# Kernel tuning notes

Measured on AMD Instinct MI355X. Metric: run time of the kernel, lower is better.

## Reference

```python
import jax, jax.numpy as jnp
import numpy as np

B, T, NODES, D = 8, 32, 400, 64   # batch graphs, time steps, stocks, node_feat_dim==lstm_dim
N = B * T * NODES                 # 102400 total nodes
E = 1_638_400                     # edges (avg degree 16)
L1, L2, FC1, FC2 = 96, 64, 128, 3

def setup_inputs() -> dict:
    key = jax.random.key(0)
    ks = jax.random.split(key, 12)
    rn = lambda k, shape, s=0.05: jax.random.normal(k, shape, jnp.float32) * s
    return {
        "x": jax.random.normal(ks[0], (N, D), jnp.float32),
        "edge_attr": jax.random.normal(ks[1], (E, 2), jnp.float32),
        "conv1_w": rn(ks[2], (D, L1)), "conv1_b": jnp.zeros((L1,), jnp.float32),
        "conv2_w": rn(ks[3], (L1, L2)), "conv2_b": jnp.zeros((L2,), jnp.float32),
        "lstm_w_ih": rn(ks[4], (4 * D, D)), "lstm_w_hh": rn(ks[5], (4 * D, D)),
        "lstm_b_ih": jnp.zeros((4 * D,), jnp.float32), "lstm_b_hh": jnp.zeros((4 * D,), jnp.float32),
        "fc1_w": rn(ks[6], (FC1, L2)), "fc1_b": jnp.zeros((FC1,), jnp.float32),
        "fc2_w": rn(ks[7], (FC2, FC1)), "fc2_b": jnp.zeros((FC2,), jnp.float32),
        "edge_index": jax.random.randint(ks[8], (2, E), 0, N, jnp.int32),
    }

def _normalize(x):
    m = x.mean(axis=0, keepdims=True)
    s = x.std(axis=0, ddof=1, keepdims=True)  # torch.std uses ddof=1
    return (x - m) / s

def _gcn(x, W, b, src, dst, ew):
    """GCNConv with edge weights: add self-loops (weight 1), symmetric norm, scatter-add."""
    n = x.shape[0]
    loops = jnp.arange(n, dtype=src.dtype)
    src2 = jnp.concatenate([src, loops])
    dst2 = jnp.concatenate([dst, loops])
    ew2 = jnp.concatenate([ew, jnp.ones((n,), ew.dtype)])
    deg = jax.ops.segment_sum(ew2, dst2, num_segments=n)
    dis = jnp.where(deg > 0, jax.lax.rsqrt(jnp.where(deg > 0, deg, 1.0)), 0.0)
    norm = dis[src2] * ew2 * dis[dst2]
    h = x @ W                                        # [N, out]
    return jax.ops.segment_sum(h[src2] * norm[:, None], dst2, num_segments=n) + b

def _lstm_last(xseq, w_ih, w_hh, b_ih, b_hh):
    """Single-layer LSTM (torch gate order i,f,g,o); returns last hidden state."""
    Bn = xseq.shape[0]
    H = w_hh.shape[1]
    xg = jnp.einsum('btd,gd->tbg', xseq, w_ih) + (b_ih + b_hh)  # [T, Bn, 4H]
    def step(carry, g_in):
        h, c = carry
        g = g_in + h @ w_hh.T
        i, f, gg, o = jnp.split(g, 4, axis=-1)
        c = jax.nn.sigmoid(f) * c + jax.nn.sigmoid(i) * jnp.tanh(gg)
        h = jax.nn.sigmoid(o) * jnp.tanh(c)
        return (h, c), None
    init = (jnp.zeros((Bn, H), xseq.dtype), jnp.zeros((Bn, H), xseq.dtype))
    (h, _), _ = jax.lax.scan(step, init, xg)
    return h

def reference(x, edge_attr, conv1_w, conv1_b, conv2_w, conv2_b,
              lstm_w_ih, lstm_w_hh, lstm_b_ih, lstm_b_hh,
              fc1_w, fc1_b, fc2_w, fc2_b, edge_index):
    xn = _normalize(x)
    ew = jnp.abs(edge_attr[:, 0])        # args.edgetype = 0
    src, dst = edge_index[0], edge_index[1]
    # (first LSTM over raw x in the original is dead code: output immediately overwritten)
    h = jax.nn.relu(_gcn(xn, conv1_w, conv1_b, src, dst, ew))
    h = jax.nn.relu(_gcn(h, conv2_w, conv2_b, src, dst, ew))
    # to_dense_batch (batch-contiguous nodes) + reshape/permute into per-node time series
    h = h.reshape(B, T, NODES, L2).transpose(0, 2, 1, 3).reshape(B * NODES, T, L2)
    h = _lstm_last(h, lstm_w_ih, lstm_w_hh, lstm_b_ih, lstm_b_hh)   # [B*NODES, L2]
    h = jax.nn.relu(h @ fc1_w.T + fc1_b)
    logits = h @ fc2_w.T + fc2_b
    p = jax.nn.softmax(logits, axis=1)   # softmax over class dim of 2D tensor
    return p.reshape(B, NODES, FC2)
```

## Files before the change

kernel.cpp:

```cpp
#include <hip/hip_runtime.h>
#include <hip/hip_bf16.h>
#include <hip/hip_fp16.h>

#define NN 102400
#define DD 64
#define EE 1638400
#define L1C 96
#define L2C 64
#define TT 32
#define NODESC 400
#define BB 8
#define SS 3200
#define G4 256

#define NBUK 400
#define BCAP 5120
#define PCHUNK 2048
#define NPART (EE / PCHUNK)
#define PTHR 512
#define EPT (PCHUNK / PTHR)

#define OFF_ENT  ((size_t)0)
#define OFF_A1   ((size_t)4096000)
#define OFF_G1   ((size_t)10649600)
#define OFF_ENT2 ((size_t)26214400)
#define OFF_H2   ((size_t)26214400)
#define OFF_G2   ((size_t)32768000)
#define OFF_GCUR ((size_t)39321600)
#define OFF_DIS  ((size_t)39328000)
#define OFF_RNG  ((size_t)39430400)
#define OFF_HL   ((size_t)39635200)
#define OFF_ST   ((size_t)39840000)

typedef __attribute__((ext_vector_type(8))) _Float16 f16x8;
typedef __attribute__((ext_vector_type(4))) float f32x4;

__device__ __forceinline__ void fma4(float4& a, float s, const float4& w) {
    a.x = fmaf(s, w.x, a.x); a.y = fmaf(s, w.y, a.y);
    a.z = fmaf(s, w.z, a.z); a.w = fmaf(s, w.w, a.w);
}
__device__ __forceinline__ float rcp_f(float x) { return __builtin_amdgcn_rcpf(x); }
__device__ __forceinline__ float sigm_f(float x) {
    x = fminf(fmaxf(x, -30.f), 30.f);
    return rcp_f(1.f + __expf(-x));
}
__device__ __forceinline__ float tanh_f(float x) {
    x = fminf(fmaxf(x, -15.f), 15.f);
    float e = __expf(2.f * x);
    return (e - 1.f) * rcp_f(e + 1.f);
}
__device__ __forceinline__ unsigned short f32_bf16_rtne(float f) {
    unsigned int u = __float_as_uint(f);
    unsigned int r = u + 0x7fffu + ((u >> 16) & 1u);
    return (unsigned short)(r >> 16);
}
__device__ __forceinline__ float bf16_f32(unsigned short h) {
    return __uint_as_float(((unsigned int)h) << 16);
}
__device__ __forceinline__ float4 unp4(uint2 p) {
    float4 v;
    v.x = __uint_as_float(p.x << 16);
    v.y = __uint_as_float(p.x & 0xffff0000u);
    v.z = __uint_as_float(p.y << 16);
    v.w = __uint_as_float(p.y & 0xffff0000u);
    return v;
}
__device__ __forceinline__ uint2 pk4(float4 v) {
    unsigned int u0 = ((unsigned int)f32_bf16_rtne(v.y) << 16) | f32_bf16_rtne(v.x);
    unsigned int u1 = ((unsigned int)f32_bf16_rtne(v.w) << 16) | f32_bf16_rtne(v.z);
    return make_uint2(u0, u1);
}
__device__ __forceinline__ uint2 pkh4(float4 v) {
    __half2 h0 = __floats2half2_rn(v.x, v.y);
    __half2 h1 = __floats2half2_rn(v.z, v.w);
    uint2 r;
    r.x = *(unsigned int*)&h0;
    r.y = *(unsigned int*)&h1;
    return r;
}
__device__ __forceinline__ float4 uph4(uint2 p) {
    __half2 h0 = *(__half2*)&p.x;
    __half2 h1 = *(__half2*)&p.y;
    float2 f0 = __half22float2(h0), f1 = __half22float2(h1);
    return make_float4(f0.x, f0.y, f1.x, f1.y);
}

__global__ void init_zero(int* gcur, float* st) {
    int idx = blockIdx.x * 256 + threadIdx.x;
    if (idx < NBUK * 16) gcur[idx] = 0;
    if (blockIdx.x == 0 && threadIdx.x < 128) st[threadIdx.x] = 0.f;
}

__global__ __launch_bounds__(256) void col_sums(const float* __restrict__ x, float* __restrict__ st) {
    int c = threadIdx.x & 63;
    size_t i = (size_t)blockIdx.x * 256 + threadIdx.x;
    size_t stride = (size_t)gridDim.x * 256;
    float s = 0.f, q = 0.f;
    for (size_t e = i; e < (size_t)NN * 64; e += stride) {
        float v = x[e]; s += v; q = fmaf(v, v, q);
    }
    __shared__ float ls[128];
    if (threadIdx.x < 128) ls[threadIdx.x] = 0.f;
    __syncthreads();
    atomicAdd(&ls[c], s); atomicAdd(&ls[64 + c], q);
    __syncthreads();
    if (threadIdx.x < 128) atomicAdd(&st[threadIdx.x], ls[threadIdx.x]);
}

__global__ void finalize_stats(float* st) {
    int c = threadIdx.x;
    if (c < 64) {
        float s = st[c], q = st[64 + c];
        float mean = s / (float)NN;
        float var = (q - s * s / (float)NN) / (float)(NN - 1);
        st[128 + c] = mean;
        st[192 + c] = rsqrtf(fmaxf(var, 1e-20f));
    }
}

__global__ __launch_bounds__(256) void xnd_kernel(const float* __restrict__ x, const float* __restrict__ st,
                                                  const float* __restrict__ dis, uint2* __restrict__ xnd) {
    size_t i = (size_t)blockIdx.x * 256 + threadIdx.x;
    int n = (int)(i >> 4), q = (int)(i & 15);
    float4 v = ((const float4*)x)[i];
    float4 mean4 = ((const float4*)(st + 128))[q];
    float4 istd4 = ((const float4*)(st + 192))[q];
    float dn = dis[n];
    v.x = (v.x - mean4.x) * istd4.x * dn;
    v.y = (v.y - mean4.y) * istd4.y * dn;
    v.z = (v.z - mean4.z) * istd4.z * dn;
    v.w = (v.w - mean4.w) * istd4.w * dn;
    xnd[i] = pk4(v);
}

__global__ __launch_bounds__(PTHR) void part_kernel(const int* __restrict__ ei, const float* __restrict__ ea,
                                                    int* __restrict__ gcur, int2* __restrict__ ent2) {
    __shared__ int lhist[NBUK];
    __shared__ int lofs[NBUK];
    __shared__ int lbase[NBUK];
    __shared__ int scn[PTHR];
    __shared__ int2 stage[PCHUNK];
    __shared__ int  gdst[PCHUNK];
    const int tid = threadIdx.x;
    const int e0 = blockIdx.x * PCHUNK;
    for (int i = tid; i < NBUK; i += PTHR) lhist[i] = 0;
    __syncthreads();
    int   dv[EPT]; int sv[EPT]; float wvv[EPT];
    #pragma unroll
    for (int i = 0; i < EPT; ++i) {
        int e = e0 + i * PTHR + tid;
        dv[i]  = ei[EE + e];
        sv[i]  = ei[e];
        wvv[i] = fabsf(ea[2 * (size_t)e]);
        atomicAdd(&lhist[dv[i] >> 8], 1);
    }
    __syncthreads();
    scn[tid] = (tid < NBUK) ? lhist[tid] : 0;
    __syncthreads();
    for (int d = 1; d < PTHR; d <<= 1) {
        int t = (tid >= d) ? scn[tid - d] : 0;
        __syncthreads();
        scn[tid] += t;
        __syncthreads();
    }
    if (tid < NBUK) {
        lofs[tid]  = scn[tid] - lhist[tid];
        lbase[tid] = atomicAdd(&gcur[tid * 16], lhist[tid]);
        lhist[tid] = 0;
    }
    __syncthreads();
    #pragma unroll
    for (int i = 0; i < EPT; ++i) {
        int d = dv[i];
        int b = d >> 8;
        int li = atomicAdd(&lhist[b], 1);
        int pos = lofs[b] + li;
        stage[pos] = make_int2(sv[i] | ((d & 255) << 24), __float_as_int(wvv[i]));
        int gp_ = lbase[b] + li;
        gdst[pos] = (gp_ < BCAP) ? (b * BCAP + gp_) : -1;
    }
    __syncthreads();
    for (int i = tid; i < PCHUNK; i += PTHR) {
        int g = gdst[i];
        if (g >= 0) ent2[g] = stage[i];
    }
}

__global__ __launch_bounds__(256) void bucket_csr(const int2* __restrict__ ent2, const int* __restrict__ gcur,
                                                  int2* __restrict__ ent, int2* __restrict__ rng,
                                                  float* __restrict__ dis) {
    __shared__ int nhist[256];
    __shared__ int scn[256];
    __shared__ float wsum[256];
    __shared__ int pcur[256];
    const int tid = threadIdx.x;
    const int b = blockIdx.x;
    const int base = b * BCAP;
    int cnt = gcur[b * 16];
    if (cnt > BCAP) cnt = BCAP;
    nhist[tid] = 0;
    wsum[tid] = 0.f;
    __syncthreads();
    for (int e = tid; e < cnt; e += 256) {
        int2 en = ent2[base + e];
        int dl = ((unsigned)en.x) >> 24;
        atomicAdd(&nhist[dl], 1);
        atomicAdd(&wsum[dl], __int_as_float(en.y));
    }
    __syncthreads();
    int c = nhist[tid];
    scn[tid] = c;
    __syncthreads();
    for (int d = 1; d < 256; d <<= 1) {
        int t = (tid >= d) ? scn[tid - d] : 0;
        __syncthreads();
        scn[tid] += t;
        __syncthreads();
    }
    int ps = scn[tid] - c;
    rng[b * 256 + tid] = make_int2(base + ps, base + ps + c);
    dis[b * 256 + tid] = rsqrtf(1.f + wsum[tid]);
    pcur[tid] = ps;
    __syncthreads();
    for (int e = tid; e < cnt; e += 256) {
        int2 en = ent2[base + e];
        int dl = ((unsigned)en.x) >> 24;
        int local = atomicAdd(&pcur[dl], 1);
        ent[base + local] = make_int2(en.x & 0xFFFFFF, en.y);
    }
}

#define G1_LD 72
__global__ __launch_bounds__(192) void gemm1_mfma(const unsigned short* __restrict__ A,
                                                  const float* __restrict__ Wm,
                                                  unsigned short* __restrict__ Cm) {
    __shared__ __align__(16) _Float16 As[64 * G1_LD];
    const int tid  = threadIdx.x;
    const int lane = tid & 63;
    const int wv   = tid >> 6;
    const int n15  = lane & 15;
    const int quad = lane >> 4;
    const size_t row0 = (size_t)blockIdx.x * 64;

    f16x8 wh[2][2], wl[2][2];
    #pragma unroll
    for (int t = 0; t < 2; ++t) {
        const int col = (wv + 3 * t) * 16 + n15;
        #pragma unroll
        for (int kc = 0; kc < 2; ++kc) {
            #pragma unroll
            for (int j = 0; j < 8; ++j) {
                float w = Wm[(size_t)(kc * 32 + quad * 8 + j) * 96 + col];
                _Float16 h = (_Float16)w;
                wh[t][kc][j] = h;
                wl[t][kc][j] = (_Float16)((w - (float)h) * 2048.f);
            }
        }
    }

    for (int i = tid; i < 64 * 16; i += 192) {
        int r = i >> 4, c4 = i & 15;
        uint2 p = *(const uint2*)(A + (row0 + r) * 64 + c4 * 4);
        *(uint2*)(As + r * G1_LD + c4 * 4) = p;
    }
    __syncthreads();

    f32x4 acc[2][4], accl[2][4];
    #pragma unroll
    for (int t = 0; t < 2; ++t)
        #pragma unroll
        for (int rt = 0; rt < 4; ++rt) {
            acc[t][rt]  = (f32x4){0.f, 0.f, 0.f, 0.f};
            accl[t][rt] = (f32x4){0.f, 0.f, 0.f, 0.f};
        }
    #pragma unroll
    for (int kc = 0; kc < 2; ++kc) {
        #pragma unroll
        for (int rt = 0; rt < 4; ++rt) {
            f16x8 a = *(const f16x8*)(As + (rt * 16 + n15) * G1_LD + kc * 32 + quad * 8);
            #pragma unroll
            for (int t = 0; t < 2; ++t) {
                acc[t][rt]  = __builtin_amdgcn_mfma_f32_16x16x32_f16(a, wh[t][kc], acc[t][rt],  0, 0, 0);
                accl[t][rt] = __builtin_amdgcn_mfma_f32_16x16x32_f16(a, wl[t][kc], accl[t][rt], 0, 0, 0);
            }
        }
    }
    #pragma unroll
    for (int t = 0; t < 2; ++t) {
        const int col = (wv + 3 * t) * 16 + n15;
        #pragma unroll
        for (int rt = 0; rt < 4; ++rt) {
            f32x4 c = acc[t][rt] + accl[t][rt] * (1.f / 2048.f);
            #pragma unroll
            for (int r = 0; r < 4; ++r) {
                size_t row = row0 + rt * 16 + quad * 4 + r;
                ((_Float16*)Cm)[row * 96 + col] = (_Float16)c[r];
            }
        }
    }
}

#define G2_LD 104
__global__ __launch_bounds__(256) void gemm2_mfma(const unsigned short* __restrict__ A,
                                                  const float* __restrict__ Wm,
                                                  const float* __restrict__ bin,
                                                  const float* __restrict__ dscale,
                                                  unsigned short* __restrict__ Cm) {
    __shared__ __align__(16) _Float16 As[64 * G2_LD];
    __shared__ float ds[64];
    const int tid  = threadIdx.x;
    const int lane = tid & 63;
    const int wv   = tid >> 6;
    const int n15  = lane & 15;
    const int quad = lane >> 4;
    const size_t row0 = (size_t)blockIdx.x * 64;

    f16x8 wh[3], wl[3];
    {
        const int col = wv * 16 + n15;
        #pragma unroll
        for (int kc = 0; kc < 3; ++kc) {
            #pragma unroll
            for (int j = 0; j < 8; ++j) {
                float w = Wm[(size_t)(kc * 32 + quad * 8 + j) * 64 + col];
                _Float16 h = (_Float16)w;
                wh[kc][j] = h;
                wl[kc][j] = (_Float16)((w - (float)h) * 2048.f);
            }
        }
    }
    if (tid < 64) ds[tid] = dscale[row0 + tid];

    for (int i = tid; i < 64 * 24; i += 256) {
        int r = i / 24, c4 = i % 24;
        uint2 p = *(const uint2*)(A + (row0 + r) * 96 + c4 * 4);
        float4 v = uph4(p);
        float4 b = *(const float4*)(bin + c4 * 4);
        v.x = fmaxf(v.x + b.x, 0.f); v.y = fmaxf(v.y + b.y, 0.f);
        v.z = fmaxf(v.z + b.z, 0.f); v.w = fmaxf(v.w + b.w, 0.f);
        *(uint2*)(As + r * G2_LD + c4 * 4) = pkh4(v);
    }
    __syncthreads();

    f32x4 acc[4], accl[4];
    #pragma unroll
    for (int rt = 0; rt < 4; ++rt) {
        acc[rt]  = (f32x4){0.f, 0.f, 0.f, 0.f};
        accl[rt] = (f32x4){0.f, 0.f, 0.f, 0.f};
    }
    #pragma unroll
    for (int kc = 0; kc < 3; ++kc) {
        #pragma unroll
        for (int rt = 0; rt < 4; ++rt) {
            f16x8 a = *(const f16x8*)(As + (rt * 16 + n15) * G2_LD + kc * 32 + quad * 8);
            acc[rt]  = __builtin_amdgcn_mfma_f32_16x16x32_f16(a, wh[kc], acc[rt],  0, 0, 0);
            accl[rt] = __builtin_amdgcn_mfma_f32_16x16x32_f16(a, wl[kc], accl[rt], 0, 0, 0);
        }
    }
    const int col = wv * 16 + n15;
    #pragma unroll
    for (int rt = 0; rt < 4; ++rt) {
        f32x4 c = acc[rt] + accl[rt] * (1.f / 2048.f);
        #pragma unroll
        for (int r = 0; r < 4; ++r) {
            int row = rt * 16 + quad * 4 + r;
            float v = c[r] * ds[row];
            Cm[(row0 + row) * 64 + col] = f32_bf16_rtne(v);
        }
    }
}

template<int C4>
__global__ __launch_bounds__(256) void gcn_gather(const uint2* __restrict__ h, const int2* __restrict__ rng,
                                                  const int2* __restrict__ ent, const float* __restrict__ dis,
                                                  unsigned short* __restrict__ g) {
    unsigned int idx = blockIdx.x * 256 + threadIdx.x;
    unsigned int n = idx / C4, q = idx % C4;
    float4 acc = unp4(h[(size_t)n * C4 + q]);
    int2 r = rng[n];
    int e = r.x;
    for (; e + 8 <= r.y; e += 8) {
        int2 en0 = ent[e],     en1 = ent[e + 1], en2 = ent[e + 2], en3 = ent[e + 3];
        int2 en4 = ent[e + 4], en5 = ent[e + 5], en6 = ent[e + 6], en7 = ent[e + 7];
        uint2 v0 = h[(size_t)en0.x * C4 + q];
        uint2 v1 = h[(size_t)en1.x * C4 + q];
        uint2 v2 = h[(size_t)en2.x * C4 + q];
        uint2 v3 = h[(size_t)en3.x * C4 + q];
        uint2 v4 = h[(size_t)en4.x * C4 + q];
        uint2 v5 = h[(size_t)en5.x * C4 + q];
        uint2 v6 = h[(size_t)en6.x * C4 + q];
        uint2 v7 = h[(size_t)en7.x * C4 + q];
        fma4(acc, __int_as_float(en0.y), unp4(v0));
        fma4(acc, __int_as_float(en1.y), unp4(v1));
        fma4(acc, __int_as_float(en2.y), unp4(v2));
        fma4(acc, __int_as_float(en3.y), unp4(v3));
        fma4(acc, __int_as_float(en4.y), unp4(v4));
        fma4(acc, __int_as_float(en5.y), unp4(v5));
        fma4(acc, __int_as_float(en6.y), unp4(v6));
        fma4(acc, __int_as_float(en7.y), unp4(v7));
    }
    for (; e + 4 <= r.y; e += 4) {
        int2 en0 = ent[e], en1 = ent[e + 1], en2 = ent[e + 2], en3 = ent[e + 3];
        uint2 v0 = h[(size_t)en0.x * C4 + q];
        uint2 v1 = h[(size_t)en1.x * C4 + q];
        uint2 v2 = h[(size_t)en2.x * C4 + q];
        uint2 v3 = h[(size_t)en3.x * C4 + q];
        fma4(acc, __int_as_float(en0.y), unp4(v0));
        fma4(acc, __int_as_float(en1.y), unp4(v1));
        fma4(acc, __int_as_float(en2.y), unp4(v2));
        fma4(acc, __int_as_float(en3.y), unp4(v3));
    }
    for (; e < r.y; ++e) {
        int2 en = ent[e];
        uint2 v = h[(size_t)en.x * C4 + q];
        fma4(acc, __int_as_float(en.y), unp4(v));
    }
    float dn = dis[n];
    acc.x *= dn; acc.y *= dn; acc.z *= dn; acc.w *= dn;
    *(uint2*)(g + (size_t)n * (C4 * 4) + q * 4) = pkh4(acc);
}

#define XP_LD 72
#define HP_LD2 72
#define GP_LD 258

__global__ __launch_bounds__(512, 1) void lstm_kernel(
    const __half* __restrict__ g2, const float* __restrict__ cb2,
    const float* __restrict__ whh, const float* __restrict__ wih,
    const float* __restrict__ bih, const float* __restrict__ bhh,
    float* __restrict__ hlast)
{
    __shared__ __align__(16) _Float16 xpack[32 * 16 * XP_LD];
    __shared__ __align__(16) _Float16 hhi[16 * HP_LD2];
    __shared__ __align__(16) _Float16 hlo[16 * HP_LD2];
    __shared__ float gp[16 * GP_LD];
    const int tid  = threadIdx.x;
    const int lane = tid & 63;
    const int wv   = tid >> 6;
    const int n15  = lane & 15;
    const int quad = lane >> 4;
    const int ja   = lane;

    f16x8 whh_h[2][2], whh_l[2][2], wih_h[2][2], wih_l[2][2];
    #pragma unroll
    for (int tl = 0; tl < 2; ++tl) {
        const int gate = (wv + 8 * tl) * 16 + n15;
        const float* wp = whh + (size_t)gate * 64 + quad * 8;
        const float* xp = wih + (size_t)gate * 64 + quad * 8;
        #pragma unroll
        for (int kc = 0; kc < 2; ++kc) {
            #pragma unroll
            for (int j = 0; j < 8; ++j) {
                float w = wp[kc * 32 + j];
                _Float16 h = (_Float16)w;
                whh_h[tl][kc][j] = h;
                whh_l[tl][kc][j] = (_Float16)((w - (float)h) * 2048.f);
                float v = xp[kc * 32 + j];
                _Float16 g = (_Float16)v;
                wih_h[tl][kc][j] = g;
                wih_l[tl][kc][j] = (_Float16)((v - (float)g) * 2048.f);
            }
        }
    }

    const float bi_i = bih[ja]        + bhh[ja];
    const float bi_f = bih[64 + ja]   + bhh[64 + ja];
    const float bi_g = bih[128 + ja]  + bhh[128 + ja];
    const float bi_o = bih[192 + ja]  + bhh[192 + ja];

    {
        const int s0 = blockIdx.x * 16;
        const int b_ = s0 / NODESC;
        const int node0 = s0 - b_ * NODESC;
        const int r  = (tid >> 4) & 15;
        const int c4 = tid & 15;
        const int t0 = tid >> 8;
        float4 bias4 = *(const float4*)(cb2 + c4 * 4);
        _Float16* dst = xpack + r * XP_LD + c4 * 4;
        const __half* src = g2 + ((size_t)(b_ * TT + t0) * NODESC + node0 + r) * 64 + c4 * 4;
        #pragma unroll
        for (int i = 0; i < 16; ++i) {
            uint2 p = *(const uint2*)(src + (size_t)i * 2 * NODESC * 64);
            float4 v = uph4(p);
            v.x = fmaxf(v.x + bias4.x, 0.f);
            v.y = fmaxf(v.y + bias4.y, 0.f);
            v.z = fmaxf(v.z + bias4.z, 0.f);
            v.w = fmaxf(v.w + bias4.w, 0.f);
            *(uint2*)(dst + (size_t)(t0 + i * 2) * (16 * XP_LD)) = pkh4(v);
        }
    }

    for (int i = tid; i < 16 * HP_LD2; i += 512) { hhi[i] = (_Float16)0.f; hlo[i] = (_Float16)0.f; }
    float cA_reg = 0.f, hA = 0.f;
    float cB_reg = 0.f, hB = 0.f;
    __syncthreads();

    const int xbase = n15 * XP_LD + quad * 8;
    const int hbase = n15 * HP_LD2 + quad * 8;

    for (int t = 0; t < TT; ++t) {
        f32x4 cmA  = {0.f,0.f,0.f,0.f}, clA0 = {0.f,0.f,0.f,0.f}, clA1 = {0.f,0.f,0.f,0.f};
        f32x4 cmB  = {0.f,0.f,0.f,0.f}, clB0 = {0.f,0.f,0.f,0.f}, clB1 = {0.f,0.f,0.f,0.f};
        const _Float16* xrow = xpack + (size_t)t * (16 * XP_LD);
        {
            f16x8 ax0 = *(const f16x8*)(xrow + xbase);
            f16x8 ah0 = *(const f16x8*)(hhi + hbase);
            f16x8 al0 = *(const f16x8*)(hlo + hbase);
            f16x8 ax1 = *(const f16x8*)(xrow + xbase + 32);
            f16x8 ah1 = *(const f16x8*)(hhi + hbase + 32);
            f16x8 al1 = *(const f16x8*)(hlo + hbase + 32);
            cmA  = __builtin_amdgcn_mfma_f32_16x16x32_f16(ax0, wih_h[0][0], cmA,  0, 0, 0);
            cmB  = __builtin_amdgcn_mfma_f32_16x16x32_f16(ax0, wih_h[1][0], cmB,  0, 0, 0);
            clA0 = __builtin_amdgcn_mfma_f32_16x16x32_f16(ax0, wih_l[0][0], clA0, 0, 0, 0);
            clB0 = __builtin_amdgcn_mfma_f32_16x16x32_f16(ax0, wih_l[1][0], clB0, 0, 0, 0);
            clA1 = __builtin_amdgcn_mfma_f32_16x16x32_f16(ax1, wih_l[0][1], clA1, 0, 0, 0);
            clB1 = __builtin_amdgcn_mfma_f32_16x16x32_f16(ax1, wih_l[1][1], clB1, 0, 0, 0);
            cmA  = __builtin_amdgcn_mfma_f32_16x16x32_f16(ah0, whh_h[0][0], cmA,  0, 0, 0);
            cmB  = __builtin_amdgcn_mfma_f32_16x16x32_f16(ah0, whh_h[1][0], cmB,  0, 0, 0);
            clA0 = __builtin_amdgcn_mfma_f32_16x16x32_f16(al0, whh_h[0][0], clA0, 0, 0, 0);
            clB0 = __builtin_amdgcn_mfma_f32_16x16x32_f16(al0, whh_h[1][0], clB0, 0, 0, 0);
            clA1 = __builtin_amdgcn_mfma_f32_16x16x32_f16(al1, whh_h[0][1], clA1, 0, 0, 0);
            clB1 = __builtin_amdgcn_mfma_f32_16x16x32_f16(al1, whh_h[1][1], clB1, 0, 0, 0);
            cmA  = __builtin_amdgcn_mfma_f32_16x16x32_f16(ax1, wih_h[0][1], cmA,  0, 0, 0);
            cmB  = __builtin_amdgcn_mfma_f32_16x16x32_f16(ax1, wih_h[1][1], cmB,  0, 0, 0);
            clA0 = __builtin_amdgcn_mfma_f32_16x16x32_f16(ah0, whh_l[0][0], clA0, 0, 0, 0);
            clB0 = __builtin_amdgcn_mfma_f32_16x16x32_f16(ah0, whh_l[1][0], clB0, 0, 0, 0);
            clA1 = __builtin_amdgcn_mfma_f32_16x16x32_f16(ah1, whh_l[0][1], clA1, 0, 0, 0);
            clB1 = __builtin_amdgcn_mfma_f32_16x16x32_f16(ah1, whh_l[1][1], clB1, 0, 0, 0);
            cmA  = __builtin_amdgcn_mfma_f32_16x16x32_f16(ah1, whh_h[0][1], cmA,  0, 0, 0);
            cmB  = __builtin_amdgcn_mfma_f32_16x16x32_f16(ah1, whh_h[1][1], cmB,  0, 0, 0);
        }
        f32x4 cA = cmA + (clA0 + clA1) * (1.f / 2048.f);
        f32x4 cB = cmB + (clB0 + clB1) * (1.f / 2048.f);
        #pragma unroll
        for (int r = 0; r < 4; ++r) {
            gp[(quad * 4 + r) * GP_LD + wv * 16 + n15]       = cA[r];
            gp[(quad * 4 + r) * GP_LD + (wv + 8) * 16 + n15] = cB[r];
        }
        __syncthreads();

        {
            const int qa = wv;
            float gi = gp[qa * GP_LD + ja]        + bi_i;
            float gf = gp[qa * GP_LD + 64 + ja]   + bi_f;
            float gg = gp[qa * GP_LD + 128 + ja]  + bi_g;
            float go = gp[qa * GP_LD + 192 + ja]  + bi_o;
            cA_reg = sigm_f(gf) * cA_reg + sigm_f(gi) * tanh_f(gg);
            hA = sigm_f(go) * tanh_f(cA_reg);
            _Float16 hh = (_Float16)hA;
            hhi[qa * HP_LD2 + ja] = hh;
            hlo[qa * HP_LD2 + ja] = (_Float16)((hA - (float)hh) * 2048.f);
        }
        {
            const int qa = wv + 8;
            float gi = gp[qa * GP_LD + ja]        + bi_i;
            float gf = gp[qa * GP_LD + 64 + ja]   + bi_f;
            float gg = gp[qa * GP_LD + 128 + ja]  + bi_g;
            float go = gp[qa * GP_LD + 192 + ja]  + bi_o;
            cB_reg = sigm_f(gf) * cB_reg + sigm_f(gi) * tanh_f(gg);
            hB = sigm_f(go) * tanh_f(cB_reg);
            _Float16 hh = (_Float16)hB;
            hhi[qa * HP_LD2 + ja] = hh;
            hlo[qa * HP_LD2 + ja] = (_Float16)((hB - (float)hh) * 2048.f);
        }
        __syncthreads();
    }
    hlast[((size_t)blockIdx.x * 16 + wv) * 64 + ja]     = hA;
    hlast[((size_t)blockIdx.x * 16 + wv + 8) * 64 + ja] = hB;
}

__global__ __launch_bounds__(128) void head_kernel(const float* __restrict__ hl,
                                                   const float* __restrict__ w1, const float* __restrict__ b1,
                                                   const float* __restrict__ w2, const float* __restrict__ b2,
                                                   float* __restrict__ out) {
    __shared__ float hrow[64];
    __shared__ float a1[128];
    __shared__ float lg[3];
    int s = blockIdx.x, tid = threadIdx.x;
    if (tid < 64) hrow[tid] = hl[(size_t)s * 64 + tid];
    __syncthreads();
    {
        const float4* wr = (const float4*)(w1 + (size_t)tid * 64);
        const float4* hq = (const float4*)hrow;
        float4 acc = make_float4(0.f, 0.f, 0.f, 0.f);
        #pragma unroll
        for (int k = 0; k < 16; ++k) {
            float4 wv = wr[k]; float4 hv = hq[k];
            acc.x = fmaf(wv.x, hv.x, acc.x); acc.y = fmaf(wv.y, hv.y, acc.y);
            acc.z = fmaf(wv.z, hv.z, acc.z); acc.w = fmaf(wv.w, hv.w, acc.w);
        }
        a1[tid] = fmaxf((acc.x + acc.y) + (acc.z + acc.w) + b1[tid], 0.f);
    }
    __syncthreads();
    if (tid < 3) {
        const float4* wr = (const float4*)(w2 + (size_t)tid * 128);
        const float4* aq = (const float4*)a1;
        float4 acc = make_float4(0.f, 0.f, 0.f, 0.f);
        #pragma unroll
        for (int k = 0; k < 32; ++k) {
            float4 wv = wr[k]; float4 av = aq[k];
            acc.x = fmaf(wv.x, av.x, acc.x); acc.y = fmaf(wv.y, av.y, acc.y);
            acc.z = fmaf(wv.z, av.z, acc.z); acc.w = fmaf(wv.w, av.w, acc.w);
        }
        lg[tid] = (acc.x + acc.y) + (acc.z + acc.w) + b2[tid];
    }
    __syncthreads();
    if (tid == 0) {
        float m = fmaxf(lg[0], fmaxf(lg[1], lg[2]));
        float e0 = __expf(lg[0] - m), e1 = __expf(lg[1] - m), e2 = __expf(lg[2] - m);
        float inv = 1.f / (e0 + e1 + e2);
        out[(size_t)s * 3 + 0] = e0 * inv;
        out[(size_t)s * 3 + 1] = e1 * inv;
        out[(size_t)s * 3 + 2] = e2 * inv;
    }
}

extern "C" void kernel_launch(void* const* d_in, const int* in_sizes, int n_in,
                              void* d_out, int out_size, void* d_ws, size_t ws_size,
                              hipStream_t stream) {
    (void)in_sizes; (void)n_in; (void)out_size; (void)ws_size;
    const float* x        = (const float*)d_in[0];
    const float* ea       = (const float*)d_in[1];
    const float* conv1_w  = (const float*)d_in[2];
    const float* conv1_b  = (const float*)d_in[3];
    const float* conv2_w  = (const float*)d_in[4];
    const float* conv2_b  = (const float*)d_in[5];
    const float* w_ih     = (const float*)d_in[6];
    const float* w_hh     = (const float*)d_in[7];
    const float* b_ih     = (const float*)d_in[8];
    const float* b_hh     = (const float*)d_in[9];
    const float* fc1_w    = (const float*)d_in[10];
    const float* fc1_b    = (const float*)d_in[11];
    const float* fc2_w    = (const float*)d_in[12];
    const float* fc2_b    = (const float*)d_in[13];
    const int*   ei       = (const int*)d_in[14];
    float* out = (float*)d_out;

    float* W    = (float*)d_ws;
    int2*  ent  = (int2*)(W + OFF_ENT);
    unsigned short* a1h = (unsigned short*)(W + OFF_A1);
    unsigned short* g1h = (unsigned short*)(W + OFF_G1);
    int2*  ent2 = (int2*)(W + OFF_ENT2);
    uint2* xnd  = (uint2*)(W + OFF_ENT2);
    float* h2   = W + OFF_H2;
    unsigned short* g2h = (unsigned short*)(W + OFF_G2);
    int*   gcur = (int*)(W + OFF_GCUR);
    float* dis  = W + OFF_DIS;
    int2*  rng  = (int2*)(W + OFF_RNG);
    float* hl   = W + OFF_HL;
    float* st   = W + OFF_ST;

    init_zero<<<26, 256, 0, stream>>>(gcur, st);
    col_sums<<<1024, 256, 0, stream>>>(x, st);
    finalize_stats<<<1, 64, 0, stream>>>(st);

    part_kernel<<<NPART, PTHR, 0, stream>>>(ei, ea, gcur, ent2);
    bucket_csr<<<NBUK, 256, 0, stream>>>(ent2, gcur, ent, rng, dis);

    xnd_kernel<<<NN * 16 / 256, 256, 0, stream>>>(x, st, dis, xnd);

    gcn_gather<16><<<NN * 16 / 256, 256, 0, stream>>>(xnd, rng, ent, dis, a1h);
    gemm1_mfma<<<NN / 64, 192, 0, stream>>>(a1h, conv1_w, g1h);

    gemm2_mfma<<<NN / 64, 256, 0, stream>>>(g1h, conv2_w, conv1_b, dis, (unsigned short*)h2);
    gcn_gather<16><<<NN * 16 / 256, 256, 0, stream>>>((const uint2*)h2, rng, ent, dis, g2h);

    lstm_kernel<<<SS / 16, 512, 0, stream>>>((const __half*)g2h, conv2_b, w_hh, w_ih,
                                             b_ih, b_hh, hl);

    head_kernel<<<SS, 128, 0, stream>>>(hl, fc1_w, fc1_b, fc2_w, fc2_b, out);
}
```

Baseline: 342.2 us.

## Fuse first GCN gather with both conv GEMMs in one kernel

Replaces the separate first gather, gemm1 and gemm2 kernels with one kernel per 64-node tile. The tile gathers neighbour features into shared memory, runs the conv1 MFMA with bias and ReLU into shared memory, then runs the conv2 MFMA and writes the scaled bf16 output. This removes two kernel launches and the global round trips of the a1 and g1 intermediates. In exchange the gather now runs with only 1600 blocks of 256 threads, with extra register pressure from preloaded weights and LDS use. That could lower occupancy and latency hiding for the irregular gather.

```diff
diff --git a/kernel.cpp b/kernel.cpp
--- a/kernel.cpp
+++ b/kernel.cpp
@@ -24,7 +24,6 @@
 #define OFF_A1   ((size_t)4096000)
 #define OFF_G1   ((size_t)10649600)
 #define OFF_ENT2 ((size_t)26214400)
-#define OFF_H2   ((size_t)26214400)
 #define OFF_G2   ((size_t)32768000)
 #define OFF_GCUR ((size_t)39321600)
 #define OFF_DIS  ((size_t)39328000)
@@ -231,82 +230,15 @@
 }
 
 #define G1_LD 72
-__global__ __launch_bounds__(192) void gemm1_mfma(const unsigned short* __restrict__ A,
-                                                  const float* __restrict__ Wm,
-                                                  unsigned short* __restrict__ Cm) {
+#define G2_LD 104
+__global__ __launch_bounds__(256) void fused_gcn1(
+    const uint2* __restrict__ xnd, const int2* __restrict__ rng,
+    const int2* __restrict__ ent, const float* __restrict__ dis,
+    const float* __restrict__ W1, const float* __restrict__ b1v,
+    const float* __restrict__ W2, unsigned short* __restrict__ h2out)
+{
     __shared__ __align__(16) _Float16 As[64 * G1_LD];
-    const int tid  = threadIdx.x;
-    const int lane = tid & 63;
-    const int wv   = tid >> 6;
-    const int n15  = lane & 15;
-    const int quad = lane >> 4;
-    const size_t row0 = (size_t)blockIdx.x * 64;
-
-    f16x8 wh[2][2], wl[2][2];
-    #pragma unroll
-    for (int t = 0; t < 2; ++t) {
-        const int col = (wv + 3 * t) * 16 + n15;
-        #pragma unroll
-        for (int kc = 0; kc < 2; ++kc) {
-            #pragma unroll
-            for (int j = 0; j < 8; ++j) {
-                float w = Wm[(size_t)(kc * 32 + quad * 8 + j) * 96 + col];
-                _Float16 h = (_Float16)w;
-                wh[t][kc][j] = h;
-                wl[t][kc][j] = (_Float16)((w - (float)h) * 2048.f);
-            }
-        }
-    }
-
-    for (int i = tid; i < 64 * 16; i += 192) {
-        int r = i >> 4, c4 = i & 15;
-        uint2 p = *(const uint2*)(A + (row0 + r) * 64 + c4 * 4);
-        *(uint2*)(As + r * G1_LD + c4 * 4) = p;
-    }
-    __syncthreads();
-
-    f32x4 acc[2][4], accl[2][4];
-    #pragma unroll
-    for (int t = 0; t < 2; ++t)
-        #pragma unroll
-        for (int rt = 0; rt < 4; ++rt) {
-            acc[t][rt]  = (f32x4){0.f, 0.f, 0.f, 0.f};
-            accl[t][rt] = (f32x4){0.f, 0.f, 0.f, 0.f};
-        }
-    #pragma unroll
-    for (int kc = 0; kc < 2; ++kc) {
-        #pragma unroll
-        for (int rt = 0; rt < 4; ++rt) {
-            f16x8 a = *(const f16x8*)(As + (rt * 16 + n15) * G1_LD + kc * 32 + quad * 8);
-            #pragma unroll
-            for (int t = 0; t < 2; ++t) {
-                acc[t][rt]  = __builtin_amdgcn_mfma_f32_16x16x32_f16(a, wh[t][kc], acc[t][rt],  0, 0, 0);
-                accl[t][rt] = __builtin_amdgcn_mfma_f32_16x16x32_f16(a, wl[t][kc], accl[t][rt], 0, 0, 0);
-            }
-        }
-    }
-    #pragma unroll
-    for (int t = 0; t < 2; ++t) {
-        const int col = (wv + 3 * t) * 16 + n15;
-        #pragma unroll
-        for (int rt = 0; rt < 4; ++rt) {
-            f32x4 c = acc[t][rt] + accl[t][rt] * (1.f / 2048.f);
-            #pragma unroll
-            for (int r = 0; r < 4; ++r) {
-                size_t row = row0 + rt * 16 + quad * 4 + r;
-                ((_Float16*)Cm)[row * 96 + col] = (_Float16)c[r];
-            }
-        }
-    }
-}
-
-#define G2_LD 104
-__global__ __launch_bounds__(256) void gemm2_mfma(const unsigned short* __restrict__ A,
-                                                  const float* __restrict__ Wm,
-                                                  const float* __restrict__ bin,
-                                                  const float* __restrict__ dscale,
-                                                  unsigned short* __restrict__ Cm) {
-    __shared__ __align__(16) _Float16 As[64 * G2_LD];
+    __shared__ __align__(16) _Float16 G1s[64 * G2_LD];
     __shared__ float ds[64];
     const int tid  = threadIdx.x;
     const int lane = tid & 63;
@@ -315,57 +247,158 @@
     const int quad = lane >> 4;
     const size_t row0 = (size_t)blockIdx.x * 64;
 
-    f16x8 wh[3], wl[3];
+    if (tid < 64) ds[tid] = dis[row0 + tid];
+
+    const int nt1 = (wv < 2) ? 2 : 1;
+    f16x8 w1h[2][2], w1l[2][2];
+    float b1c[2] = {0.f, 0.f};
+    #pragma unroll
+    for (int t = 0; t < 2; ++t) {
+        if (t < nt1) {
+            const int col = (wv + 4 * t) * 16 + n15;
+            b1c[t] = b1v[col];
+            #pragma unroll
+            for (int kc = 0; kc < 2; ++kc) {
+                #pragma unroll
+                for (int j = 0; j < 8; ++j) {
+                    float w = W1[(size_t)(kc * 32 + quad * 8 + j) * 96 + col];
+                    _Float16 h = (_Float16)w;
+                    w1h[t][kc][j] = h;
+                    w1l[t][kc][j] = (_Float16)((w - (float)h) * 2048.f);
+                }
+            }
+        }
+    }
+    f16x8 w2h[3], w2l[3];
     {
         const int col = wv * 16 + n15;
         #pragma unroll
         for (int kc = 0; kc < 3; ++kc) {
             #pragma unroll
             for (int j = 0; j < 8; ++j) {
-                float w = Wm[(size_t)(kc * 32 + quad * 8 + j) * 64 + col];
+                float w = W2[(size_t)(kc * 32 + quad * 8 + j) * 64 + col];
                 _Float16 h = (_Float16)w;
-                wh[kc][j] = h;
-                wl[kc][j] = (_Float16)((w - (float)h) * 2048.f);
+                w2h[kc][j] = h;
+                w2l[kc][j] = (_Float16)((w - (float)h) * 2048.f);
             }
         }
     }
-    if (tid < 64) ds[tid] = dscale[row0 + tid];
-
-    for (int i = tid; i < 64 * 24; i += 256) {
-        int r = i / 24, c4 = i % 24;
-        uint2 p = *(const uint2*)(A + (row0 + r) * 96 + c4 * 4);
-        float4 v = uph4(p);
-        float4 b = *(const float4*)(bin + c4 * 4);
-        v.x = fmaxf(v.x + b.x, 0.f); v.y = fmaxf(v.y + b.y, 0.f);
-        v.z = fmaxf(v.z + b.z, 0.f); v.w = fmaxf(v.w + b.w, 0.f);
-        *(uint2*)(As + r * G2_LD + c4 * 4) = pkh4(v);
-    }
-    __syncthreads();
-
-    f32x4 acc[4], accl[4];
-    #pragma unroll
-    for (int rt = 0; rt < 4; ++rt) {
-        acc[rt]  = (f32x4){0.f, 0.f, 0.f, 0.f};
-        accl[rt] = (f32x4){0.f, 0.f, 0.f, 0.f};
-    }
-    #pragma unroll
-    for (int kc = 0; kc < 3; ++kc) {
+
+    for (int u = 0; u < 4; ++u) {
+        int idx = u * 256 + tid;
+        int nl = idx >> 4, q = idx & 15;
+        size_t n = row0 + nl;
+        float4 acc = unp4(xnd[n * 16 + q]);
+        int2 r = rng[n];
+        int e = r.x;
+        for (; e + 8 <= r.y; e += 8) {
+            int2 en0 = ent[e],     en1 = ent[e + 1], en2 = ent[e + 2], en3 = ent[e + 3];
+            int2 en4 = ent[e + 4], en5 = ent[e + 5], en6 = ent[e + 6], en7 = ent[e + 7];
+            uint2 v0 = xnd[(size_t)en0.x * 16 + q];
+            uint2 v1 = xnd[(size_t)en1.x * 16 + q];
+            uint2 v2 = xnd[(size_t)en2.x * 16 + q];
+            uint2 v3 = xnd[(size_t)en3.x * 16 + q];
+            uint2 v4 = xnd[(size_t)en4.x * 16 + q];
+            uint2 v5 = xnd[(size_t)en5.x * 16 + q];
+            uint2 v6 = xnd[(size_t)en6.x * 16 + q];
+            uint2 v7 = xnd[(size_t)en7.x * 16 + q];
+            fma4(acc, __int_as_float(en0.y), unp4(v0));
+            fma4(acc, __int_as_float(en1.y), unp4(v1));
+            fma4(acc, __int_as_float(en2.y), unp4(v2));
+            fma4(acc, __int_as_float(en3.y), unp4(v3));
+            fma4(acc, __int_as_float(en4.y), unp4(v4));
+            fma4(acc, __int_as_float(en5.y), unp4(v5));
+            fma4(acc, __int_as_float(en6.y), unp4(v6));
+            fma4(acc, __int_as_float(en7.y), unp4(v7));
+        }
+        for (; e + 4 <= r.y; e += 4) {
+            int2 en0 = ent[e], en1 = ent[e + 1], en2 = ent[e + 2], en3 = ent[e + 3];
+            uint2 v0 = xnd[(size_t)en0.x * 16 + q];
+            uint2 v1 = xnd[(size_t)en1.x * 16 + q];
+            uint2 v2 = xnd[(size_t)en2.x * 16 + q];
+            uint2 v3 = xnd[(size_t)en3.x * 16 + q];
+            fma4(acc, __int_as_float(en0.y), unp4(v0));
+            fma4(acc, __int_as_float(en1.y), unp4(v1));
+            fma4(acc, __int_as_float(en2.y), unp4(v2));
+            fma4(acc, __int_as_float(en3.y), unp4(v3));
+        }
+        for (; e < r.y; ++e) {
+            int2 en = ent[e];
+            uint2 v = xnd[(size_t)en.x * 16 + q];
+            fma4(acc, __int_as_float(en.y), unp4(v));
+        }
+        float dn = dis[n];
+        acc.x *= dn; acc.y *= dn; acc.z *= dn; acc.w *= dn;
+        *(uint2*)(As + nl * G1_LD + q * 4) = pkh4(acc);
+    }
+    __syncthreads();
+
+    {
+        f32x4 acc1[2][4], accl1[2][4];
+        #pragma unroll
+        for (int t = 0; t < 2; ++t)
+            #pragma unroll
+            for (int rt = 0; rt < 4; ++rt) {
+                acc1[t][rt]  = (f32x4){0.f, 0.f, 0.f, 0.f};
+                accl1[t][rt] = (f32x4){0.f, 0.f, 0.f, 0.f};
+            }
+        #pragma unroll
+        for (int kc = 0; kc < 2; ++kc) {
+            #pragma unroll
+            for (int rt = 0; rt < 4; ++rt) {
+                f16x8 a = *(const f16x8*)(As + (rt * 16 + n15) * G1_LD + kc * 32 + quad * 8);
+                acc1[0][rt]  = __builtin_amdgcn_mfma_f32_16x16x32_f16(a, w1h[0][kc], acc1[0][rt],  0, 0, 0);
+                accl1[0][rt] = __builtin_amdgcn_mfma_f32_16x16x32_f16(a, w1l[0][kc], accl1[0][rt], 0, 0, 0);
+                if (nt1 == 2) {
+                    acc1[1][rt]  = __builtin_amdgcn_mfma_f32_16x16x32_f16(a, w1h[1][kc], acc1[1][rt],  0, 0, 0);
+                    accl1[1][rt] = __builtin_amdgcn_mfma_f32_16x16x32_f16(a, w1l[1][kc], accl1[1][rt], 0, 0, 0);
+                }
+            }
+        }
+        #pragma unroll
+        for (int t = 0; t < 2; ++t) {
+            if (t < nt1) {
+                const int col = (wv + 4 * t) * 16 + n15;
+                #pragma unroll
+                for (int rt = 0; rt < 4; ++rt) {
+                    f32x4 c = acc1[t][rt] + accl1[t][rt] * (1.f / 2048.f);
+                    #pragma unroll
+                    for (int r = 0; r < 4; ++r) {
+                        int row = rt * 16 + quad * 4 + r;
+                        G1s[row * G2_LD + col] = (_Float16)fmaxf(c[r] + b1c[t], 0.f);
+                    }
+                }
+            }
+        }
+    }
+    __syncthreads();
+
+    {
+        f32x4 acc[4], accl[4];
         #pragma unroll
         for (int rt = 0; rt < 4; ++rt) {
-            f16x8 a = *(const f16x8*)(As + (rt * 16 + n15) * G2_LD + kc * 32 + quad * 8);
-            acc[rt]  = __builtin_amdgcn_mfma_f32_16x16x32_f16(a, wh[kc], acc[rt],  0, 0, 0);
-            accl[rt] = __builtin_amdgcn_mfma_f32_16x16x32_f16(a, wl[kc], accl[rt], 0, 0, 0);
-        }
-    }
-    const int col = wv * 16 + n15;
-    #pragma unroll
-    for (int rt = 0; rt < 4; ++rt) {
-        f32x4 c = acc[rt] + accl[rt] * (1.f / 2048.f);
-        #pragma unroll
-        for (int r = 0; r < 4; ++r) {
-            int row = rt * 16 + quad * 4 + r;
-            float v = c[r] * ds[row];
-            Cm[(row0 + row) * 64 + col] = f32_bf16_rtne(v);
+            acc[rt]  = (f32x4){0.f, 0.f, 0.f, 0.f};
+            accl[rt] = (f32x4){0.f, 0.f, 0.f, 0.f};
+        }
+        #pragma unroll
+        for (int kc = 0; kc < 3; ++kc) {
+            #pragma unroll
+            for (int rt = 0; rt < 4; ++rt) {
+                f16x8 a = *(const f16x8*)(G1s + (rt * 16 + n15) * G2_LD + kc * 32 + quad * 8);
+                acc[rt]  = __builtin_amdgcn_mfma_f32_16x16x32_f16(a, w2h[kc], acc[rt],  0, 0, 0);
+                accl[rt] = __builtin_amdgcn_mfma_f32_16x16x32_f16(a, w2l[kc], accl[rt], 0, 0, 0);
+            }
+        }
+        const int col = wv * 16 + n15;
+        #pragma unroll
+        for (int rt = 0; rt < 4; ++rt) {
+            f32x4 c = acc[rt] + accl[rt] * (1.f / 2048.f);
+            #pragma unroll
+            for (int r = 0; r < 4; ++r) {
+                int row = rt * 16 + quad * 4 + r;
+                float v = c[r] * ds[row];
+                h2out[(row0 + row) * 64 + col] = f32_bf16_rtne(v);
+            }
         }
     }
 }
@@ -638,11 +671,9 @@
 
     float* W    = (float*)d_ws;
     int2*  ent  = (int2*)(W + OFF_ENT);
-    unsigned short* a1h = (unsigned short*)(W + OFF_A1);
-    unsigned short* g1h = (unsigned short*)(W + OFF_G1);
+    unsigned short* h2  = (unsigned short*)(W + OFF_A1);
     int2*  ent2 = (int2*)(W + OFF_ENT2);
     uint2* xnd  = (uint2*)(W + OFF_ENT2);
-    float* h2   = W + OFF_H2;
     unsigned short* g2h = (unsigned short*)(W + OFF_G2);
     int*   gcur = (int*)(W + OFF_GCUR);
     float* dis  = W + OFF_DIS;
@@ -659,10 +690,9 @@
 
     xnd_kernel<<<NN * 16 / 256, 256, 0, stream>>>(x, st, dis, xnd);
 
-    gcn_gather<16><<<NN * 16 / 256, 256, 0, stream>>>(xnd, rng, ent, dis, a1h);
-    gemm1_mfma<<<NN / 64, 192, 0, stream>>>(a1h, conv1_w, g1h);
-
-    gemm2_mfma<<<NN / 64, 256, 0, stream>>>(g1h, conv2_w, conv1_b, dis, (unsigned short*)h2);
+    fused_gcn1<<<NN / 64, 256, 0, stream>>>(xnd, rng, ent, dis,
+                                            conv1_w, conv1_b, conv2_w, h2);
+
     gcn_gather<16><<<NN * 16 / 256, 256, 0, stream>>>((const uint2*)h2, rng, ent, dis, g2h);
 
     lstm_kernel<<<SS / 16, 512, 0, stream>>>((const __half*)g2h, conv2_b, w_hh, w_ih,
```

New measurement: 368.3 us. +7.6%, slower.
